# Optimization experiments

Hardware: AMD Instinct MI355X
Metric: run time of the kernel (lower is better)

Reference implementation:

```python
import jax, jax.numpy as jnp
import numpy as np

B, N, C, H, D, K = 4, 8192, 384, 12, 2, 256
M = N // K          # 32 members per cluster
CH = C // H         # 32 head dim


def setup_inputs() -> dict:
    key = jax.random.key(0)
    ks = jax.random.split(key, 8)
    pos = jax.random.uniform(ks[0], (B, N, D), jnp.float32) * 100.0
    feat = jax.random.normal(ks[1], (B, N, C), jnp.float32)
    # each batch's points partitioned into K clusters of M members (a permutation)
    perms = jax.vmap(lambda kk: jax.random.permutation(kk, N))(jax.random.split(ks[2], B))
    member_idx = perms.reshape(B * K, M).astype(jnp.int32)               # z x m
    batch_idx = jnp.broadcast_to(
        jnp.repeat(jnp.arange(B, dtype=jnp.int32), K)[:, None], (B * K, M))
    w = 0.02
    qkv_w = jax.random.normal(ks[3], (3 * C, C), jnp.float32) * w
    qkv_b = jnp.zeros((3 * C,), jnp.float32)
    pos_w = jax.random.normal(ks[4], (H, D), jnp.float32) * w
    pos_b = jnp.zeros((H,), jnp.float32)
    proj_w = jax.random.normal(ks[5], (C, C), jnp.float32) * w
    proj_b = jnp.zeros((C,), jnp.float32)
    return dict(pos=pos, feat=feat, member_idx=member_idx, batch_idx=batch_idx,
                qkv_w=qkv_w, qkv_b=qkv_b, pos_w=pos_w, pos_b=pos_b,
                proj_w=proj_w, proj_b=proj_b, k=K)


def reference(pos, feat, member_idx, batch_idx, qkv_w, qkv_b, pos_w, pos_b,
              proj_w, proj_b, k):
    # attend_means=True, mask=None, cluster_score=None, q_subsample_idx=None path
    b, n, c = feat.shape
    d = pos.shape[2]
    h = pos_w.shape[0]
    ch = c // h
    z, m = member_idx.shape
    scale = ch ** -0.5

    qkv = feat @ qkv_w.T + qkv_b            # b,n,3c
    q = qkv[..., :c]                        # b,n,c
    kv = qkv[..., c:]                       # b,n,2c

    pos_orig = pos
    pos_n = pos / jnp.max(pos.reshape(-1, d), axis=0)   # per-coordinate max norm

    # irregular gather of kv / pos per cluster member
    kv_g = kv[batch_idx, member_idx]        # z,m,2c
    pos_g = pos_n[batch_idx, member_idx]    # z,m,d

    # cluster_score=None, mask=None -> uniform weights 1/m (mean over members)
    kv_mean = jnp.mean(kv_g, axis=1).reshape(b, k, 2, h, ch)
    pos_mean = jnp.mean(pos_g, axis=1).reshape(b, k, d)

    key_ = kv_mean[:, :, 0].transpose(0, 2, 1, 3)   # b,h,k,ch
    v = kv_mean[:, :, 1].transpose(0, 2, 1, 3)      # b,h,k,ch
    qh = q.reshape(b, n, h, ch).transpose(0, 2, 1, 3) * scale  # b,h,n,ch

    attn = jnp.einsum('bhnc,bhkc->bhnk', qh, key_)  # b,h,n,k
    rel_pos = pos_mean[:, None, :, :] - pos_orig[:, :, None, :]  # b,n,k,d
    pos_bias = jnp.einsum('bnkd,hd->bhnk', rel_pos, pos_w) + pos_b[None, :, None, None]
    attn = jax.nn.softmax(attn + pos_bias, axis=-1)

    out = jnp.einsum('bhnk,bhkc->bnhc', attn, v).reshape(b, n, c)
    return out @ proj_w.T + proj_b
```

## Files before the change

kernel.cpp:

```cpp
#include <hip/hip_runtime.h>

typedef __attribute__((ext_vector_type(8))) short bf16x8;
typedef __attribute__((ext_vector_type(4))) float f32x4;

#define MFMA16(a,b,c) __builtin_amdgcn_mfma_f32_16x16x32_bf16((a),(b),(c),0,0,0)

__device__ __forceinline__ float b2f(unsigned short u){
  union { unsigned u; float f; } x; x.u = ((unsigned)u) << 16; return x.f;
}
__device__ __forceinline__ unsigned short f2b(float f){
  union { float f; unsigned u; } x; x.f = f;
  unsigned r = x.u + 0x7FFFu + ((x.u >> 16) & 1u);
  return (unsigned short)(r >> 16);
}
__device__ __forceinline__ unsigned pk_rne(float a, float b){
  unsigned ua = __float_as_uint(a), ub = __float_as_uint(b);
  ua += 0x7FFFu + ((ua >> 16) & 1u);
  ub += 0x7FFFu + ((ub >> 16) & 1u);
  return __builtin_amdgcn_perm(ub, ua, 0x07060302u);
}
__device__ __forceinline__ unsigned pk_trunc(float a, float b){
  return __builtin_amdgcn_perm(__float_as_uint(b), __float_as_uint(a), 0x07060302u);
}
__device__ __forceinline__ bf16x8 mk8(unsigned a, unsigned b, unsigned c, unsigned d){
  union { uint4 u; bf16x8 h; } x; x.u = make_uint4(a,b,c,d); return x.h;
}
__device__ __forceinline__ int permp(int cl){
  return (cl & 0xE0) | (((cl >> 2) & 3) << 3) | (((cl >> 4) & 1) << 2) | (cl & 3);
}

typedef __attribute__((address_space(3))) unsigned int lds_u32;
typedef const __attribute__((address_space(1))) unsigned int glb_u32;
__device__ __forceinline__ void gl_lds16(const void* g, void* l){
  __builtin_amdgcn_global_load_lds((glb_u32*)g, (lds_u32*)l, 16, 0, 0);
}

__global__ __launch_bounds__(192) void prep_means_kernel(
    const float* __restrict__ pos, unsigned* __restrict__ pmax,
    const float* __restrict__ qkv_w, unsigned short* __restrict__ qkvwb,
    const float* __restrict__ proj_w, unsigned short* __restrict__ projwb,
    const float* __restrict__ feat,
    const int* __restrict__ member_idx, const int* __restrict__ batch_idx,
    unsigned short* __restrict__ fm, float* __restrict__ pm,
    unsigned short* __restrict__ featb)
{
  int bid = blockIdx.x, t = threadIdx.x;
  if (bid < 1024){
    int g = t / 96, tl = t - g*96;
    int z = bid;
    __shared__ int bases[32];
    __shared__ float4 part[96];
    if (t < 32) bases[t] = batch_idx[z*32 + t]*8192 + member_idx[z*32 + t];
    __syncthreads();
    if (t < 32){
      float2 pp = ((const float2*)pos)[bases[t]];
      #pragma unroll
      for (int off = 16; off >= 1; off >>= 1){
        pp.x += __shfl_xor(pp.x, off, 32);
        pp.y += __shfl_xor(pp.y, off, 32);
      }
      if (t == 0){ pm[z*2] = pp.x*(1.f/32.f); pm[z*2+1] = pp.y*(1.f/32.f); }
    }
    float4 v[16]; int rows[16];
    const float4* f4 = (const float4*)feat;
    #pragma unroll
    for (int m = 0; m < 16; m++){
      rows[m] = bases[g*16 + m];
      v[m] = f4[(long)rows[m]*96 + tl];
    }
    float4 a = {0.f,0.f,0.f,0.f};
    #pragma unroll
    for (int m = 0; m < 16; m++){
      *(uint2*)(featb + (long)rows[m]*384 + tl*4) =
          make_uint2(pk_rne(v[m].x, v[m].y), pk_rne(v[m].z, v[m].w));
      a.x += v[m].x; a.y += v[m].y; a.z += v[m].z; a.w += v[m].w;
    }
    if (g == 1) part[tl] = a;
    __syncthreads();
    if (g == 0){
      float4 b = part[tl];
      a.x += b.x; a.y += b.y; a.z += b.z; a.w += b.w;
      unsigned d0 = pk_rne(a.x*(1.f/32.f), a.y*(1.f/32.f));
      unsigned d1 = pk_rne(a.z*(1.f/32.f), a.w*(1.f/32.f));
      *(uint2*)(fm + (long)z*384 + tl*4) = make_uint2(d0, d1);
    }
  } else if (bid < 1408){
    int u = (bid - 1024)*192 + t;
    const float* in; unsigned short* o; long i;
    if (u < 55296){ in = qkv_w;  o = qkvwb;  i = u; }
    else          { in = proj_w; o = projwb; i = u - 55296; }
    const float4* p = (const float4*)(in + i*8);
    float4 a = p[0], b = p[1];
    *(uint4*)(o + i*8) = make_uint4(pk_rne(a.x,a.y), pk_rne(a.z,a.w),
                                    pk_rne(b.x,b.y), pk_rne(b.z,b.w));
  } else {
    int i = (bid - 1408)*192 + t;
    if (i < 16384){
      float4 v = ((const float4*)pos)[i];
      float m0 = fmaxf(v.x, v.z), m1 = fmaxf(v.y, v.w);
      #pragma unroll
      for (int off = 32; off >= 1; off >>= 1){
        m0 = fmaxf(m0, __shfl_xor(m0, off, 64));
        m1 = fmaxf(m1, __shfl_xor(m1, off, 64));
      }
      if ((t & 63) == 0){
        atomicMax(&pmax[0], __float_as_uint(m0));
        atomicMax(&pmax[1], __float_as_uint(m1));
      }
    }
  }
}

__global__ __launch_bounds__(512) void kvq_kernel(
    const unsigned short* __restrict__ fm,
    const unsigned short* __restrict__ featb,
    const unsigned short* __restrict__ qkvwb,
    const float* __restrict__ qkv_b,
    const float* __restrict__ pm, const float* __restrict__ pmaxf,
    const float* __restrict__ pos_w, const float* __restrict__ pos_b,
    unsigned short* __restrict__ kh, unsigned short* __restrict__ vt,
    unsigned short* __restrict__ wt,
    unsigned short* __restrict__ q_s, float q_scale)
{
  __shared__ unsigned short As[64*64];
  __shared__ unsigned short Ws[384*64];
  __shared__ unsigned short wtS[256];
  const int K = 384;
  int tid = threadIdx.x;
  int lane = tid & 63, wave = tid >> 6;
  int l15 = lane & 15, quad = lane >> 4;
  int sw = l15 & 7;
  int srow = tid >> 3, sc8 = tid & 7;

  if (blockIdx.x < 96){
    int mt = blockIdx.x / 6, nt = blockIdx.x - mt*6;
    int m0 = mt << 6, n0 = nt << 7;
    int b = m0 >> 8, cl0 = m0 & 255;
    const unsigned short* W = qkvwb + 384*384;
    if (nt >= 3 && tid < 256){
      int lh = tid >> 6, lc = tid & 63;
      int h = ((n0 - 384) >> 5) + lh;
      int cl = cl0 + lc;
      float p0 = pm[(b*256 + cl)*2]   / pmaxf[0];
      float p1 = pm[(b*256 + cl)*2+1] / pmaxf[1];
      float bias = p0*pos_w[h*2] + p1*pos_w[h*2+1] + pos_b[h];
      unsigned short wv = f2b(exp2f(bias * 1.44269504088896340f));
      wtS[lh*64 + lc] = wv;
      wt[(((long)(b*12 + h)) << 8) + permp(cl)] = wv;
    }
    int wr = (wave >> 2) << 5, wc = (wave & 3) << 5;
    f32x4 acc[2][2];
    #pragma unroll
    for (int i = 0; i < 2; i++)
      #pragma unroll
      for (int j = 0; j < 2; j++) acc[i][j] = (f32x4){0.f,0.f,0.f,0.f};

    for (int k0 = 0; k0 < K; k0 += 64){
      __syncthreads();
      int gc8 = sc8 ^ (srow & 7);
      gl_lds16(fm + (long)(m0+srow)*K + k0 + gc8*8, As + wave*512);
      #pragma unroll
      for (int it = 0; it < 2; it++){
        int r = it*64 + srow;
        int g2 = sc8 ^ (r & 7);
        gl_lds16(W + (long)(n0+r)*K + k0 + g2*8, Ws + it*4096 + wave*512);
      }
      __syncthreads();
      #pragma unroll
      for (int kk = 0; kk < 2; kk++){
        bf16x8 af[2], bfr[2];
        #pragma unroll
        for (int i = 0; i < 2; i++)
          af[i] = *(const bf16x8*)(As + (wr + i*16 + l15)*64 + (((kk<<2)+quad) ^ sw)*8);
        #pragma unroll
        for (int j = 0; j < 2; j++)
          bfr[j] = *(const bf16x8*)(Ws + (wc + j*16 + l15)*64 + (((kk<<2)+quad) ^ sw)*8);
        #pragma unroll
        for (int i = 0; i < 2; i++)
          #pragma unroll
          for (int j = 0; j < 2; j++)
            acc[i][j] = MFMA16(af[i], bfr[j], acc[i][j]);
      }
    }

    #pragma unroll
    for (int j = 0; j < 2; j++){
      int col = n0 + wc + j*16 + l15;
      float bv = qkv_b[384 + col];
      #pragma unroll
      for (int i = 0; i < 2; i++){
        #pragma unroll
        for (int r = 0; r < 4; r++){
          float v = acc[i][j][r] + bv;
          int lr = wr + i*16 + quad*4 + r;
          int cl = cl0 + lr;
          if (col < 384){
            int h = col >> 5, ch = col & 31;
            kh[((((long)b*12 + h)*256 + cl)*32) + ch] = f2b(v);
          } else {
            int cn = col - 384;
            int h = cn >> 5, ch = cn & 31;
            int pp = permp(cl);
            int c8 = (pp >> 3) ^ (ch & 7);
            float w = b2f(wtS[(wave & 3)*64 + lr]);
            vt[(((long)b*12 + h)*32 + ch)*256 + c8*8 + (pp & 7)] = f2b(v * w);
          }
        }
      }
    }
  } else {
    int m0 = (blockIdx.x - 96) << 6;
    f32x4 acc[4][3];
    #pragma unroll
    for (int i = 0; i < 4; i++)
      #pragma unroll
      for (int j = 0; j < 3; j++) acc[i][j] = (f32x4){0.f,0.f,0.f,0.f};

    for (int k0 = 0; k0 < K; k0 += 64){
      __syncthreads();
      int gc8 = sc8 ^ (srow & 7);
      gl_lds16(featb + (long)(m0+srow)*K + k0 + gc8*8, As + wave*512);
      #pragma unroll
      for (int it = 0; it < 6; it++){
        int r = it*64 + srow;
        int g2 = sc8 ^ (r & 7);
        gl_lds16(qkvwb + (long)r*K + k0 + g2*8, Ws + it*4096 + wave*512);
      }
      __syncthreads();
      #pragma unroll
      for (int kk = 0; kk < 2; kk++){
        bf16x8 af[4];
        #pragma unroll
        for (int i = 0; i < 4; i++)
          af[i] = *(const bf16x8*)(As + (i*16 + l15)*64 + (((kk<<2)+quad) ^ sw)*8);
        #pragma unroll
        for (int j = 0; j < 3; j++){
          bf16x8 bfr = *(const bf16x8*)(Ws + (wave*48 + j*16 + l15)*64 + (((kk<<2)+quad) ^ sw)*8);
          #pragma unroll
          for (int i = 0; i < 4; i++)
            acc[i][j] = MFMA16(af[i], bfr, acc[i][j]);
        }
      }
    }

    #pragma unroll
    for (int j = 0; j < 3; j++){
      int col = wave*48 + j*16 + l15;
      float bv = qkv_b[col];
      #pragma unroll
      for (int i = 0; i < 4; i++){
        int row0 = m0 + i*16 + quad*4;
        #pragma unroll
        for (int r = 0; r < 4; r++){
          float v = (acc[i][j][r] + bv) * q_scale;
          int row = row0 + r;
          int bb = row >> 13, tok = row & 8191;
          q_s[((((long)(bb*12 + (col >> 5))) << 13) + tok)*32 + (col & 31)] = f2b(v);
        }
      }
    }
  }
}

__global__ __launch_bounds__(512) void gemm_proj_kernel(
    const unsigned short* __restrict__ A, const unsigned short* __restrict__ W,
    const float* __restrict__ bias, float* __restrict__ C)
{
  __shared__ unsigned short As[64*64];
  __shared__ unsigned short Ws[384*64];
  const int K = 384, N = 384;
  int m0 = blockIdx.x << 6;
  int tid = threadIdx.x;
  int lane = tid & 63, wave = tid >> 6;
  int l15 = lane & 15, quad = lane >> 4;
  int sw = l15 & 7;
  int srow = tid >> 3, sc8 = tid & 7;

  f32x4 acc[4][3];
  #pragma unroll
  for (int i = 0; i < 4; i++)
    #pragma unroll
    for (int j = 0; j < 3; j++) acc[i][j] = (f32x4){0.f,0.f,0.f,0.f};

  for (int k0 = 0; k0 < K; k0 += 64){
    __syncthreads();
    {
      int gc8 = sc8 ^ (srow & 7);
      int row = m0 + srow;
      int bb = row >> 13, tok = row & 8191;
      int ch = k0 + gc8*8;
      const unsigned short* asrc = A + ((((long)(bb*12 + (ch >> 5))) << 13) + tok)*32 + (ch & 31);
      gl_lds16(asrc, As + wave*512);
    }
    #pragma unroll
    for (int it = 0; it < 6; it++){
      int r = it*64 + srow;
      int g2 = sc8 ^ (r & 7);
      gl_lds16(W + (long)r*K + k0 + g2*8, Ws + it*4096 + wave*512);
    }
    __syncthreads();
    #pragma unroll
    for (int kk = 0; kk < 2; kk++){
      bf16x8 af[4];
      #pragma unroll
      for (int i = 0; i < 4; i++)
        af[i] = *(const bf16x8*)(As + (i*16 + l15)*64 + (((kk<<2)+quad) ^ sw)*8);
      #pragma unroll
      for (int j = 0; j < 3; j++){
        bf16x8 bfr = *(const bf16x8*)(Ws + (wave*48 + j*16 + l15)*64 + (((kk<<2)+quad) ^ sw)*8);
        #pragma unroll
        for (int i = 0; i < 4; i++)
          acc[i][j] = MFMA16(af[i], bfr, acc[i][j]);
      }
    }
  }

  #pragma unroll
  for (int j = 0; j < 3; j++){
    int col = wave*48 + j*16 + l15;
    float bv = bias[col];
    #pragma unroll
    for (int i = 0; i < 4; i++){
      int row0 = m0 + i*16 + quad*4;
      #pragma unroll
      for (int r = 0; r < 4; r++)
        C[(long)(row0 + r)*N + col] = acc[i][j][r] + bv;
    }
  }
}

__global__ __launch_bounds__(256) void attn_kernel(
    const unsigned short* __restrict__ qhm,
    const unsigned short* __restrict__ kh,
    const unsigned short* __restrict__ vt,
    const unsigned short* __restrict__ wt,
    unsigned short* __restrict__ aohm)
{
  __shared__ unsigned short keyS[256*32];
  __shared__ unsigned short vTS[32*256];
  __shared__ unsigned short wS[256];

  int bid = blockIdx.x;
  int chunk = bid & 63;
  int bh = bid >> 6;
  int n0 = chunk << 7;
  int tid = threadIdx.x, lane = tid & 63, wave = tid >> 6;
  int l15 = lane & 15, quad = lane >> 4;
  int sw = l15 & 7;

  const unsigned short* khb = kh + (long)bh*8192;
  const unsigned short* vtb = vt + (long)bh*8192;
  #pragma unroll
  for (int it = 0; it < 4; it++){
    gl_lds16(khb + it*2048 + tid*8, keyS + it*2048 + wave*512);
    gl_lds16(vtb + it*2048 + tid*8, vTS  + it*2048 + wave*512);
  }
  if (tid < 32) *(uint4*)(wS + tid*8) = *(const uint4*)(wt + ((long)bh << 8) + tid*8);

  long qbase = ((long)bh*8192 + n0 + wave*32 + l15)*32 + quad*8;
  bf16x8 aq0 = *(const bf16x8*)(qhm + qbase);
  bf16x8 aq1 = *(const bf16x8*)(qhm + qbase + 512);
  __syncthreads();

  f32x4 o00 = {0.f,0.f,0.f,0.f}, o01 = {0.f,0.f,0.f,0.f}, os0 = {0.f,0.f,0.f,0.f};
  f32x4 o10 = {0.f,0.f,0.f,0.f}, o11 = {0.f,0.f,0.f,0.f}, os1 = {0.f,0.f,0.f,0.f};
  #pragma unroll
  for (int ks = 0; ks < 8; ks++){
    bf16x8 bk0 = *(const bf16x8*)(keyS + ((2*ks  )*16 + l15)*32 + quad*8);
    bf16x8 bk1 = *(const bf16x8*)(keyS + ((2*ks+1)*16 + l15)*32 + quad*8);
    f32x4 z4 = {0.f,0.f,0.f,0.f};
    f32x4 s00 = MFMA16(bk0, aq0, z4);
    f32x4 s01 = MFMA16(bk1, aq0, z4);
    f32x4 s10 = MFMA16(bk0, aq1, z4);
    f32x4 s11 = MFMA16(bk1, aq1, z4);
    #pragma unroll
    for (int c = 0; c < 4; c++){
      s00[c] = exp2f(s00[c]); s01[c] = exp2f(s01[c]);
      s10[c] = exp2f(s10[c]); s11[c] = exp2f(s11[c]);
    }
    bf16x8 pf0 = mk8(pk_trunc(s00[0],s00[1]), pk_trunc(s00[2],s00[3]),
                     pk_trunc(s01[0],s01[1]), pk_trunc(s01[2],s01[3]));
    bf16x8 pf1 = mk8(pk_trunc(s10[0],s10[1]), pk_trunc(s10[2],s10[3]),
                     pk_trunc(s11[0],s11[1]), pk_trunc(s11[2],s11[3]));
    int c8 = (4*ks + quad) ^ sw;
    bf16x8 a0 = *(const bf16x8*)(vTS + l15*256      + c8*8);
    bf16x8 a1 = *(const bf16x8*)(vTS + (16+l15)*256 + c8*8);
    bf16x8 wf = *(const bf16x8*)(wS + ks*32 + quad*8);
    o00 = MFMA16(a0, pf0, o00);
    o01 = MFMA16(a1, pf0, o01);
    os0 = MFMA16(wf, pf0, os0);
    o10 = MFMA16(a0, pf1, o10);
    o11 = MFMA16(a1, pf1, o11);
    os1 = MFMA16(wf, pf1, os1);
  }

  float inv0 = 1.f / os0[0];
  float inv1 = 1.f / os1[0];
  long ob0 = ((long)bh*8192 + n0 + wave*32 + l15)*32 + quad*4;
  *(uint2*)(aohm + ob0)      = make_uint2(pk_rne(o00[0]*inv0, o00[1]*inv0),
                                          pk_rne(o00[2]*inv0, o00[3]*inv0));
  *(uint2*)(aohm + ob0 + 16) = make_uint2(pk_rne(o01[0]*inv0, o01[1]*inv0),
                                          pk_rne(o01[2]*inv0, o01[3]*inv0));
  long ob1 = ob0 + 512;
  *(uint2*)(aohm + ob1)      = make_uint2(pk_rne(o10[0]*inv1, o10[1]*inv1),
                                          pk_rne(o10[2]*inv1, o10[3]*inv1));
  *(uint2*)(aohm + ob1 + 16) = make_uint2(pk_rne(o11[0]*inv1, o11[1]*inv1),
                                          pk_rne(o11[2]*inv1, o11[3]*inv1));
}

extern "C" void kernel_launch(void* const* d_in, const int* in_sizes, int n_in,
                              void* d_out, int out_size, void* d_ws, size_t ws_size,
                              hipStream_t stream)
{
  const float* pos      = (const float*)d_in[0];
  const float* feat     = (const float*)d_in[1];
  const int* member_idx = (const int*)d_in[2];
  const int* batch_idx  = (const int*)d_in[3];
  const float* qkv_w    = (const float*)d_in[4];
  const float* qkv_b    = (const float*)d_in[5];
  const float* pos_w    = (const float*)d_in[6];
  const float* pos_b    = (const float*)d_in[7];
  const float* proj_w   = (const float*)d_in[8];
  const float* proj_b   = (const float*)d_in[9];
  float* out = (float*)d_out;

  char* ws = (char*)d_ws;
  float* pmax           = (float*)ws;
  float* pm             = (float*)(ws + 256);
  unsigned short* fm    = (unsigned short*)(ws + 8704);
  unsigned short* kh    = (unsigned short*)(ws + 795136);
  unsigned short* vt    = (unsigned short*)(ws + 1581568);
  unsigned short* wt    = (unsigned short*)(ws + 2368000);
  unsigned short* q_s   = (unsigned short*)(ws + 2417152);
  unsigned short* ao    = (unsigned short*)(ws + 27582976);
  unsigned short* qkvwb = (unsigned short*)(ws + 52748800);
  unsigned short* projwb= (unsigned short*)(ws + 53633536);
  unsigned short* featb = (unsigned short*)(ws + 53928448);

  hipMemsetAsync(pmax, 0, 8, stream);
  prep_means_kernel<<<1494, 192, 0, stream>>>(pos, (unsigned*)pmax, qkv_w, qkvwb,
                                              proj_w, projwb, feat, member_idx,
                                              batch_idx, fm, pm, featb);
  kvq_kernel<<<608, 512, 0, stream>>>(fm, featb, qkvwb, qkv_b, pm, pmax, pos_w, pos_b,
                                      kh, vt, wt, q_s,
                                      0.17677669529663687f * 1.44269504088896340f);
  attn_kernel<<<3072, 256, 0, stream>>>(q_s, kh, vt, wt, ao);
  gemm_proj_kernel<<<512, 512, 0, stream>>>(ao, projwb, proj_b, out);
}
```

Baseline: 192.0 us.

## Double query rows per attention block and merge KV and Q GEMM blocks

The attention kernel now handles 256 query rows per block (64 per wave, four 16-row tiles) instead of 128. This halves the grid and the number of times each block reloads the per-head key and value tiles into LDS. The fused KV/Q projection kernel drops from 608 to 512 blocks: the 96 KV blocks also each compute one Q tile afterward, so that work is spread across fewer blocks. In exchange there is more register pressure in attention, fewer blocks for latency hiding, and longer tails in the KV blocks.

```diff
diff --git a/kernel.cpp b/kernel.cpp
--- a/kernel.cpp
+++ b/kernel.cpp
@@ -132,6 +132,7 @@
   int sw = l15 & 7;
   int srow = tid >> 3, sc8 = tid & 7;
 
+  int qtile;
   if (blockIdx.x < 96){
     int mt = blockIdx.x / 6, nt = blockIdx.x - mt*6;
     int m0 = mt << 6, n0 = nt << 7;
@@ -208,8 +209,13 @@
         }
       }
     }
+    qtile = 416 + blockIdx.x;
   } else {
-    int m0 = (blockIdx.x - 96) << 6;
+    qtile = blockIdx.x - 96;
+  }
+
+  {
+    int m0 = qtile << 6;
     f32x4 acc[4][3];
     #pragma unroll
     for (int i = 0; i < 4; i++)
@@ -341,9 +347,9 @@
   __shared__ unsigned short wS[256];
 
   int bid = blockIdx.x;
-  int chunk = bid & 63;
-  int bh = bid >> 6;
-  int n0 = chunk << 7;
+  int chunk = bid & 31;
+  int bh = bid >> 5;
+  int n0 = chunk << 8;
   int tid = threadIdx.x, lane = tid & 63, wave = tid >> 6;
   int l15 = lane & 15, quad = lane >> 4;
   int sw = l15 & 7;
@@ -357,55 +363,57 @@
   }
   if (tid < 32) *(uint4*)(wS + tid*8) = *(const uint4*)(wt + ((long)bh << 8) + tid*8);
 
-  long qbase = ((long)bh*8192 + n0 + wave*32 + l15)*32 + quad*8;
-  bf16x8 aq0 = *(const bf16x8*)(qhm + qbase);
-  bf16x8 aq1 = *(const bf16x8*)(qhm + qbase + 512);
+  long qbase = ((long)bh*8192 + n0 + wave*64 + l15)*32 + quad*8;
+  bf16x8 aq[4];
+  #pragma unroll
+  for (int ti = 0; ti < 4; ti++)
+    aq[ti] = *(const bf16x8*)(qhm + qbase + ti*512);
   __syncthreads();
 
-  f32x4 o00 = {0.f,0.f,0.f,0.f}, o01 = {0.f,0.f,0.f,0.f}, os0 = {0.f,0.f,0.f,0.f};
-  f32x4 o10 = {0.f,0.f,0.f,0.f}, o11 = {0.f,0.f,0.f,0.f}, os1 = {0.f,0.f,0.f,0.f};
+  f32x4 o0[4], o1[4], os[4];
+  #pragma unroll
+  for (int ti = 0; ti < 4; ti++){
+    o0[ti] = (f32x4){0.f,0.f,0.f,0.f};
+    o1[ti] = (f32x4){0.f,0.f,0.f,0.f};
+    os[ti] = (f32x4){0.f,0.f,0.f,0.f};
+  }
+
   #pragma unroll
   for (int ks = 0; ks < 8; ks++){
     bf16x8 bk0 = *(const bf16x8*)(keyS + ((2*ks  )*16 + l15)*32 + quad*8);
     bf16x8 bk1 = *(const bf16x8*)(keyS + ((2*ks+1)*16 + l15)*32 + quad*8);
-    f32x4 z4 = {0.f,0.f,0.f,0.f};
-    f32x4 s00 = MFMA16(bk0, aq0, z4);
-    f32x4 s01 = MFMA16(bk1, aq0, z4);
-    f32x4 s10 = MFMA16(bk0, aq1, z4);
-    f32x4 s11 = MFMA16(bk1, aq1, z4);
-    #pragma unroll
-    for (int c = 0; c < 4; c++){
-      s00[c] = exp2f(s00[c]); s01[c] = exp2f(s01[c]);
-      s10[c] = exp2f(s10[c]); s11[c] = exp2f(s11[c]);
-    }
-    bf16x8 pf0 = mk8(pk_trunc(s00[0],s00[1]), pk_trunc(s00[2],s00[3]),
-                     pk_trunc(s01[0],s01[1]), pk_trunc(s01[2],s01[3]));
-    bf16x8 pf1 = mk8(pk_trunc(s10[0],s10[1]), pk_trunc(s10[2],s10[3]),
-                     pk_trunc(s11[0],s11[1]), pk_trunc(s11[2],s11[3]));
+    const f32x4 z4 = {0.f,0.f,0.f,0.f};
+    bf16x8 pf[4];
+    #pragma unroll
+    for (int ti = 0; ti < 4; ti++){
+      f32x4 s0 = MFMA16(bk0, aq[ti], z4);
+      f32x4 s1 = MFMA16(bk1, aq[ti], z4);
+      #pragma unroll
+      for (int c = 0; c < 4; c++){ s0[c] = exp2f(s0[c]); s1[c] = exp2f(s1[c]); }
+      pf[ti] = mk8(pk_trunc(s0[0],s0[1]), pk_trunc(s0[2],s0[3]),
+                   pk_trunc(s1[0],s1[1]), pk_trunc(s1[2],s1[3]));
+    }
     int c8 = (4*ks + quad) ^ sw;
     bf16x8 a0 = *(const bf16x8*)(vTS + l15*256      + c8*8);
     bf16x8 a1 = *(const bf16x8*)(vTS + (16+l15)*256 + c8*8);
     bf16x8 wf = *(const bf16x8*)(wS + ks*32 + quad*8);
-    o00 = MFMA16(a0, pf0, o00);
-    o01 = MFMA16(a1, pf0, o01);
-    os0 = MFMA16(wf, pf0, os0);
-    o10 = MFMA16(a0, pf1, o10);
-    o11 = MFMA16(a1, pf1, o11);
-    os1 = MFMA16(wf, pf1, os1);
-  }
-
-  float inv0 = 1.f / os0[0];
-  float inv1 = 1.f / os1[0];
-  long ob0 = ((long)bh*8192 + n0 + wave*32 + l15)*32 + quad*4;
-  *(uint2*)(aohm + ob0)      = make_uint2(pk_rne(o00[0]*inv0, o00[1]*inv0),
-                                          pk_rne(o00[2]*inv0, o00[3]*inv0));
-  *(uint2*)(aohm + ob0 + 16) = make_uint2(pk_rne(o01[0]*inv0, o01[1]*inv0),
-                                          pk_rne(o01[2]*inv0, o01[3]*inv0));
-  long ob1 = ob0 + 512;
-  *(uint2*)(aohm + ob1)      = make_uint2(pk_rne(o10[0]*inv1, o10[1]*inv1),
-                                          pk_rne(o10[2]*inv1, o10[3]*inv1));
-  *(uint2*)(aohm + ob1 + 16) = make_uint2(pk_rne(o11[0]*inv1, o11[1]*inv1),
-                                          pk_rne(o11[2]*inv1, o11[3]*inv1));
+    #pragma unroll
+    for (int ti = 0; ti < 4; ti++){
+      o0[ti] = MFMA16(a0, pf[ti], o0[ti]);
+      o1[ti] = MFMA16(a1, pf[ti], o1[ti]);
+      os[ti] = MFMA16(wf, pf[ti], os[ti]);
+    }
+  }
+
+  #pragma unroll
+  for (int ti = 0; ti < 4; ti++){
+    float inv = 1.f / os[ti][0];
+    long ob = ((long)bh*8192 + n0 + wave*64 + ti*16 + l15)*32 + quad*4;
+    *(uint2*)(aohm + ob)      = make_uint2(pk_rne(o0[ti][0]*inv, o0[ti][1]*inv),
+                                           pk_rne(o0[ti][2]*inv, o0[ti][3]*inv));
+    *(uint2*)(aohm + ob + 16) = make_uint2(pk_rne(o1[ti][0]*inv, o1[ti][1]*inv),
+                                           pk_rne(o1[ti][2]*inv, o1[ti][3]*inv));
+  }
 }
 
 extern "C" void kernel_launch(void* const* d_in, const int* in_sizes, int n_in,
@@ -441,9 +449,9 @@
   prep_means_kernel<<<1494, 192, 0, stream>>>(pos, (unsigned*)pmax, qkv_w, qkvwb,
                                               proj_w, projwb, feat, member_idx,
                                               batch_idx, fm, pm, featb);
-  kvq_kernel<<<608, 512, 0, stream>>>(fm, featb, qkvwb, qkv_b, pm, pmax, pos_w, pos_b,
+  kvq_kernel<<<512, 512, 0, stream>>>(fm, featb, qkvwb, qkv_b, pm, pmax, pos_w, pos_b,
                                       kh, vt, wt, q_s,
                                       0.17677669529663687f * 1.44269504088896340f);
-  attn_kernel<<<3072, 256, 0, stream>>>(q_s, kh, vt, wt, ao);
+  attn_kernel<<<1536, 256, 0, stream>>>(q_s, kh, vt, wt, ao);
   gemm_proj_kernel<<<512, 512, 0, stream>>>(ao, projwb, proj_b, out);
 }
```

Result: faster. 186.8 us (-2.7%).
